# Kernel optimization log

Measured on AMD Instinct MI355X. Metric: run time of the kernel, lower is better.

## Reference

```python
import jax, jax.numpy as jnp
import numpy as np

N = 50000
E_RAND = 800000
F_IN = 128
H = 4          # num_heads
D_HID = 32     # hidden per-head dim
D_OUT = 32     # output per-head dim
NEG_SLOPE_ATTN = 0.2   # DGL GATConv attention leaky_relu
NEG_SLOPE_ACT = 0.01   # F.leaky_relu default activation


def setup_inputs() -> dict:
    key = jax.random.key(0)
    ks = jax.random.split(key, 12)
    x = jax.random.normal(ks[0], (N, F_IN), dtype=jnp.float32)
    src_r = jax.random.randint(ks[1], (E_RAND,), 0, N, dtype=jnp.int32)
    dst_r = jax.random.randint(ks[2], (E_RAND,), 0, N, dtype=jnp.int32)
    loop = jnp.arange(N, dtype=jnp.int32)
    src = jnp.concatenate([src_r, loop])  # add_self_loop
    dst = jnp.concatenate([dst_r, loop])
    sc1 = 1.0 / np.sqrt(F_IN)
    sc2 = 1.0 / np.sqrt(H * D_HID)
    W1 = jax.random.normal(ks[3], (F_IN, H * D_HID), dtype=jnp.float32) * sc1
    al1 = jax.random.normal(ks[4], (H, D_HID), dtype=jnp.float32) * sc1
    ar1 = jax.random.normal(ks[5], (H, D_HID), dtype=jnp.float32) * sc1
    b1 = jnp.zeros((H * D_HID,), dtype=jnp.float32)
    W2 = jax.random.normal(ks[6], (H * D_HID, H * D_OUT), dtype=jnp.float32) * sc2
    al2 = jax.random.normal(ks[7], (H, D_OUT), dtype=jnp.float32) * sc2
    ar2 = jax.random.normal(ks[8], (H, D_OUT), dtype=jnp.float32) * sc2
    b2 = jnp.zeros((H * D_OUT,), dtype=jnp.float32)
    return {"x": x, "src": src, "dst": dst,
            "W1": W1, "al1": al1, "ar1": ar1, "b1": b1,
            "W2": W2, "al2": al2, "ar2": ar2, "b2": b2}


def gat_conv(x, src, dst, W, al, ar, b, act_slope):
    n = x.shape[0]
    h, d = al.shape
    feat = (x @ W).reshape(n, h, d)                 # [N,H,D]
    el = jnp.einsum('nhd,hd->nh', feat, al)         # [N,H]
    er = jnp.einsum('nhd,hd->nh', feat, ar)
    # edge attention score on edge u->v: leaky_relu(el[u] + er[v])
    e = jax.nn.leaky_relu(el[src] + er[dst], NEG_SLOPE_ATTN)  # [E,H]
    # edge softmax over incoming edges of each dst node (self-loops guarantee >=1 edge)
    m = jax.ops.segment_max(e, dst, num_segments=n)           # [N,H]
    ex = jnp.exp(e - m[dst])
    s = jax.ops.segment_sum(ex, dst, num_segments=n)
    a = ex / s[dst]                                           # [E,H]
    # attention-weighted scatter-sum of source features
    out = jax.ops.segment_sum(a[:, :, None] * feat[src], dst, num_segments=n)  # [N,H,D]
    out = out + b.reshape(h, d)
    if act_slope is not None:
        out = jax.nn.leaky_relu(out, act_slope)
    return out.reshape(n, h * d)                    # flatten(1)


def reference(x, src, dst, W1, al1, ar1, b1, W2, al2, ar2, b2):
    h = gat_conv(x, src, dst, W1, al1, ar1, b1, NEG_SLOPE_ACT)
    out = gat_conv(h, src, dst, W2, al2, ar2, b2, None)  # last layer: no activation
    return out
```

## Files before the change

### kernel.cpp

```cpp
#include <hip/hip_runtime.h>
#include <hip/hip_bf16.h>
#include <hip/hip_fp16.h>

#define HEADS 4
#define DHEAD 32
#define FDIM 128
#define BCAP 64
#define RPB 64
#define XPAD (FDIM/4 + 1)
#define DEGPAD 16
#define WSTRIDE 68

typedef float nfloat4 __attribute__((ext_vector_type(4)));

__device__ __forceinline__ void gemm_body(
    const float* __restrict__ X, const float* __restrict__ W,
    const float* __restrict__ al, const float* __restrict__ ar,
    __half* __restrict__ feat, float* __restrict__ el, float* __restrict__ er,
    int n, float* Xs) {
    int r0 = blockIdx.x * RPB;
    int rowsLeft = n - r0; if (rowsLeft > RPB) rowsLeft = RPB;
    {
        nfloat4* xsw = (nfloat4*)Xs;
        const nfloat4* Xg = (const nfloat4*)(X + (size_t)r0 * FDIM);
        for (int i = threadIdx.x; i < RPB * (FDIM / 4); i += 256) {
            int row = i >> 5, c4 = i & 31;
            int sr = row < rowsLeft ? row : 0;
            xsw[row * XPAD + c4] =
                __builtin_nontemporal_load(&Xg[(size_t)sr * (FDIM / 4) + c4]);
        }
    }
    __syncthreads();

    int head = __builtin_amdgcn_readfirstlane(threadIdx.x >> 6);
    int lane = threadIdx.x & 63;
    int row = r0 + lane;
    bool valid = row < n;

    const float4* xs4 = (const float4*)Xs + (size_t)lane * XPAD;
    const float* wb = W + head * DHEAD;

    float acc[32];
#pragma unroll
    for (int j = 0; j < 32; j++) acc[j] = 0.f;

#pragma unroll 4
    for (int k4 = 0; k4 < FDIM / 4; k4++) {
        float4 a = xs4[k4];
#pragma unroll
        for (int kk = 0; kk < 4; kk++) {
            const float4* wr = (const float4*)(wb + (size_t)(k4 * 4 + kk) * FDIM);
            float s = (&a.x)[kk];
#pragma unroll
            for (int j4 = 0; j4 < 8; j4++) {
                float4 wv = wr[j4];
                acc[j4 * 4 + 0] += s * wv.x;
                acc[j4 * 4 + 1] += s * wv.y;
                acc[j4 * 4 + 2] += s * wv.z;
                acc[j4 * 4 + 3] += s * wv.w;
            }
        }
    }

    float elv = 0.f, erv = 0.f;
#pragma unroll
    for (int j = 0; j < 32; j++) {
        elv += acc[j] * al[head * DHEAD + j];
        erv += acc[j] * ar[head * DHEAD + j];
    }
    if (valid) {
        el[(size_t)row * HEADS + head] = elv;
        er[(size_t)row * HEADS + head] = erv;
    }

    if (valid) {
        union { __half2 h2[16]; uint4 u4[4]; } pk;
#pragma unroll
        for (int m = 0; m < 16; m++)
            pk.h2[m] = __floats2half2_rn(acc[2 * m], acc[2 * m + 1]);
        uint4* dstp = (uint4*)(feat + (size_t)row * FDIM + head * DHEAD);
#pragma unroll
        for (int t = 0; t < 4; t++) dstp[t] = pk.u4[t];
    }
}

__global__ __launch_bounds__(256) void k_gemm_l1(
    const float* __restrict__ X, const float* __restrict__ W,
    const float* __restrict__ al, const float* __restrict__ ar,
    __half* __restrict__ feat, float* __restrict__ el, float* __restrict__ er, int n,
    const int* __restrict__ esrc, const int* __restrict__ edst,
    int* __restrict__ degp, ushort* __restrict__ bucket, int E) {
    __shared__ float Xs[RPB * 4 * XPAD];

    {
        int nb = gridDim.x;
        int echunk = (E + nb - 1) / nb;
        int e0 = blockIdx.x * echunk;
        int e1 = e0 + echunk; if (e1 > E) e1 = E;
        for (int base = e0 + threadIdx.x; base < e1; base += 256 * 8) {
            int d[8], s[8], p[8];
#pragma unroll
            for (int j = 0; j < 8; j++) {
                int idx = base + j * 256;
                if (idx < e1) {
                    d[j] = __builtin_nontemporal_load(&edst[idx]);
                    s[j] = __builtin_nontemporal_load(&esrc[idx]);
                } else d[j] = -1;
            }
#pragma unroll
            for (int j = 0; j < 8; j++)
                if (d[j] >= 0) p[j] = atomicAdd(&degp[(size_t)d[j] * DEGPAD], 1);
#pragma unroll
            for (int j = 0; j < 8; j++)
                if (d[j] >= 0 && p[j] < BCAP)
                    bucket[((size_t)d[j] << 6) + p[j]] = (ushort)s[j];
        }
    }

    gemm_body(X, W, al, ar, feat, el, er, n, Xs);
}

__global__ __launch_bounds__(256) void k_gemm_l2(
    const float* __restrict__ X, const float* __restrict__ W,
    const float* __restrict__ al, const float* __restrict__ ar,
    __half* __restrict__ feat, float* __restrict__ el, float* __restrict__ er, int n) {
    __shared__ float Xs[RPB * 4 * XPAD];
    gemm_body(X, W, al, ar, feat, el, er, n, Xs);
}

__device__ __forceinline__ void agg_body(
    const ushort* __restrict__ bucket, const int* __restrict__ degp,
    const __half2* __restrict__ feat2h, const float* __restrict__ el,
    const float* __restrict__ er, const float* __restrict__ b,
    float* __restrict__ out, int n, int apply_act) {
    __shared__ float ws_all[4][HEADS * WSTRIDE];
    int wave = threadIdx.x >> 6;
    int node = blockIdx.x * 4 + wave;
    if (node >= n) return;
    node = __builtin_amdgcn_readfirstlane(node);
    int lane = threadIdx.x & 63;
    float* ws = ws_all[wave];

    int cnt = __builtin_amdgcn_readfirstlane(degp[(size_t)node * DEGPAD]);
    if (cnt > BCAP) cnt = BCAP;
    const ushort* bkt = bucket + ((size_t)node << 6);

    {
        int ph = lane >> 4;
        int sl = lane & 15;
        float ern = er[(size_t)node * HEADS + ph];
        int slot[4]; float ev[4];
#pragma unroll
        for (int bb = 0; bb < 4; bb++) {
            slot[bb] = bb * 16 + sl;
            int s = (int)bkt[slot[bb]];
            if (s >= n) s = 0;
            ev[bb] = el[(size_t)s * HEADS + ph];
        }
#pragma unroll
        for (int bb = 0; bb < 4; bb++) {
            float t = ev[bb] + ern;
            t = t > 0.f ? t : 0.2f * t;
            float w = (slot[bb] < cnt) ? __expf(t) : 0.f;
            ws[ph * WSTRIDE + slot[bb]] = w;
        }
    }
    asm volatile("s_waitcnt lgkmcnt(0)" ::: "memory");

    int h = lane >> 4;
    const float2* wsh2 = (const float2*)(ws + h * WSTRIDE);
    const uint* bp32 = (const uint*)bkt;
    float ax = 0.f, ay = 0.f, sw = 0.f;
    int pairs = (cnt + 1) >> 1;
    for (int k0 = 0; k0 < pairs; k0 += 4) {
        uint pk[4];
#pragma unroll
        for (int u = 0; u < 4; u++) {
            int kk = k0 + u;
            pk[u] = __builtin_amdgcn_readfirstlane(kk < pairs ? bp32[kk] : 0u);
        }
        __half2 f[8]; float2 w2[4];
#pragma unroll
        for (int u = 0; u < 4; u++) {
            int s0 = (int)(pk[u] & 0xffffu), s1 = (int)(pk[u] >> 16);
            if (s0 >= n) s0 = 0;
            if (s1 >= n) s1 = 0;
            f[2 * u]     = feat2h[(size_t)s0 * 64 + lane];
            f[2 * u + 1] = feat2h[(size_t)s1 * 64 + lane];
            w2[u] = wsh2[k0 + u];
        }
#pragma unroll
        for (int u = 0; u < 4; u++) {
            float2 f0 = __half22float2(f[2 * u]);
            float2 f1 = __half22float2(f[2 * u + 1]);
            sw += w2[u].x + w2[u].y;
            ax += w2[u].x * f0.x + w2[u].y * f1.x;
            ay += w2[u].x * f0.y + w2[u].y * f1.y;
        }
    }

    float inv = 1.0f / sw;
    float2 bv = ((const float2*)b)[lane];
    float ox = ax * inv + bv.x;
    float oy = ay * inv + bv.y;
    if (apply_act) {
        ox = ox > 0.f ? ox : 0.01f * ox;
        oy = oy > 0.f ? oy : 0.01f * oy;
    }
    float2 o; o.x = ox; o.y = oy;
    ((float2*)out)[(size_t)node * 64 + lane] = o;
}

__global__ __launch_bounds__(256) void k_agg_l1(
    const ushort* __restrict__ bucket, const int* __restrict__ degp,
    const __half2* __restrict__ feat2h, const float* __restrict__ el,
    const float* __restrict__ er, const float* __restrict__ b,
    float* __restrict__ out, int n) {
    agg_body(bucket, degp, feat2h, el, er, b, out, n, 1);
}

__global__ __launch_bounds__(256) void k_agg_l2(
    const ushort* __restrict__ bucket, const int* __restrict__ degp,
    const __half2* __restrict__ feat2h, const float* __restrict__ el,
    const float* __restrict__ er, const float* __restrict__ b,
    float* __restrict__ out, int n) {
    agg_body(bucket, degp, feat2h, el, er, b, out, n, 0);
}


extern "C" void kernel_launch(void* const* d_in, const int* in_sizes, int n_in,
                              void* d_out, int out_size, void* d_ws, size_t ws_size,
                              hipStream_t stream) {
    const float* x   = (const float*)d_in[0];
    const int*   src = (const int*)d_in[1];
    const int*   dst = (const int*)d_in[2];
    const float* W1  = (const float*)d_in[3];
    const float* al1 = (const float*)d_in[4];
    const float* ar1 = (const float*)d_in[5];
    const float* b1  = (const float*)d_in[6];
    const float* W2  = (const float*)d_in[7];
    const float* al2 = (const float*)d_in[8];
    const float* ar2 = (const float*)d_in[9];
    const float* b2  = (const float*)d_in[10];
    int N = in_sizes[0] / FDIM;
    int E = in_sizes[1];
    float* out = (float*)d_out;

    __half* featA  = (__half*)d_ws;
    float*  elb    = (float*)(featA + (size_t)N * FDIM);
    float*  erb    = elb + (size_t)N * HEADS;
    int*    degp   = (int*)(erb + (size_t)N * HEADS);
    ushort* bucket = (ushort*)(degp + (size_t)N * DEGPAD);
    float*  hbuf   = out;

    int gblocks = (N + RPB - 1) / RPB;
    int ablocks = (N + 3) / 4;

    (void)hipMemsetAsync(degp, 0, (size_t)N * DEGPAD * sizeof(int), stream);

    k_gemm_l1<<<gblocks, 256, 0, stream>>>(x, W1, al1, ar1, featA, elb, erb, N,
                                           src, dst, degp, bucket, E);
    k_agg_l1<<<ablocks, 256, 0, stream>>>(bucket, degp, (const __half2*)featA,
                                          elb, erb, b1, hbuf, N);

    k_gemm_l2<<<gblocks, 256, 0, stream>>>(hbuf, W2, al2, ar2, featA, elb, erb, N);
    k_agg_l2<<<ablocks, 256, 0, stream>>>(bucket, degp, (const __half2*)featA,
                                          elb, erb, b2, out, N);
}
```

Before: 274.5 us.

## Replace global-atomic edge bucketing with binned counting-sort pipeline

Graph construction switches from per-edge global atomics on a padded degree array to a three-pass binned counting sort. First a shared-memory histogram of destination bins, then a scan and a partition of packed (dst,src) edges into bins, then per-bin local-atomic bucket fill. The goal is to remove contended, scattered global atomics and the large memset of the padded degree array. In exchange it adds three small kernel launches and an extra pass over the edges, and it reuses the output buffer as scratch space. Packing dst in 16 bits only works because the low bits are recomputed per bin, and src must fit in 16 bits.

```diff
diff --git a/kernel.cpp b/kernel.cpp
--- a/kernel.cpp
+++ b/kernel.cpp
@@ -8,7 +8,8 @@
 #define BCAP 64
 #define RPB 64
 #define XPAD (FDIM/4 + 1)
-#define DEGPAD 16
+#define BINSH 8
+#define MAXBINS 256
 #define WSTRIDE 68
 
 typedef float nfloat4 __attribute__((ext_vector_type(4)));
@@ -88,48 +89,106 @@
     const float* __restrict__ X, const float* __restrict__ W,
     const float* __restrict__ al, const float* __restrict__ ar,
     __half* __restrict__ feat, float* __restrict__ el, float* __restrict__ er, int n,
-    const int* __restrict__ esrc, const int* __restrict__ edst,
-    int* __restrict__ degp, ushort* __restrict__ bucket, int E) {
+    const int* __restrict__ edst, int* __restrict__ bincnt, int E) {
     __shared__ float Xs[RPB * 4 * XPAD];
-
+    __shared__ int hist[MAXBINS];
+
+    for (int i = threadIdx.x; i < MAXBINS; i += 256) hist[i] = 0;
+    __syncthreads();
     {
         int nb = gridDim.x;
         int echunk = (E + nb - 1) / nb;
         int e0 = blockIdx.x * echunk;
         int e1 = e0 + echunk; if (e1 > E) e1 = E;
-        for (int base = e0 + threadIdx.x; base < e1; base += 256 * 8) {
-            int d[8], s[8], p[8];
-#pragma unroll
-            for (int j = 0; j < 8; j++) {
-                int idx = base + j * 256;
-                if (idx < e1) {
-                    d[j] = __builtin_nontemporal_load(&edst[idx]);
-                    s[j] = __builtin_nontemporal_load(&esrc[idx]);
-                } else d[j] = -1;
-            }
-#pragma unroll
-            for (int j = 0; j < 8; j++)
-                if (d[j] >= 0) p[j] = atomicAdd(&degp[(size_t)d[j] * DEGPAD], 1);
-#pragma unroll
-            for (int j = 0; j < 8; j++)
-                if (d[j] >= 0 && p[j] < BCAP)
-                    bucket[((size_t)d[j] << 6) + p[j]] = (ushort)s[j];
-        }
+        for (int idx = e0 + threadIdx.x; idx < e1; idx += 256)
+            atomicAdd(&hist[__builtin_nontemporal_load(&edst[idx]) >> BINSH], 1);
+        __syncthreads();
+        int hv = hist[threadIdx.x];
+        if (threadIdx.x < MAXBINS && hv) atomicAdd(&bincnt[threadIdx.x], hv);
     }
 
     gemm_body(X, W, al, ar, feat, el, er, n, Xs);
 }
 
-__global__ __launch_bounds__(256) void k_gemm_l2(
-    const float* __restrict__ X, const float* __restrict__ W,
-    const float* __restrict__ al, const float* __restrict__ ar,
-    __half* __restrict__ feat, float* __restrict__ el, float* __restrict__ er, int n) {
-    __shared__ float Xs[RPB * 4 * XPAD];
-    gemm_body(X, W, al, ar, feat, el, er, n, Xs);
+__global__ __launch_bounds__(256) void k_scan(
+    const int* __restrict__ bincnt, int* __restrict__ binbase,
+    int* __restrict__ cursor, int nbins) {
+    __shared__ int sb[MAXBINS];
+    int tid = threadIdx.x;
+    int v0 = (tid < nbins) ? bincnt[tid] : 0;
+    sb[tid] = v0;
+    __syncthreads();
+    for (int off = 1; off < MAXBINS; off <<= 1) {
+        int t = 0;
+        if (tid >= off) t = sb[tid - off];
+        __syncthreads();
+        if (tid >= off) sb[tid] += t;
+        __syncthreads();
+    }
+    int excl = sb[tid] - v0;
+    if (tid < nbins) { binbase[tid] = excl; cursor[tid] = excl; }
+    if (tid == 0) binbase[nbins] = sb[MAXBINS - 1];
+}
+
+__global__ __launch_bounds__(256) void k_p2(
+    const int* __restrict__ esrc, const int* __restrict__ edst,
+    int* __restrict__ cursor, uint* __restrict__ ebin, int E, int nbins) {
+    __shared__ int lcnt[MAXBINS];
+    __shared__ int lbase[MAXBINS];
+    int tid = threadIdx.x;
+    for (int i = tid; i < MAXBINS; i += 256) lcnt[i] = 0;
+    __syncthreads();
+    int nb = gridDim.x;
+    int echunk = (E + nb - 1) / nb;
+    int e0 = blockIdx.x * echunk;
+    int e1 = e0 + echunk; if (e1 > E) e1 = E;
+    int d[5], s[5], lo[5], bb[5];
+    bool v[5];
+#pragma unroll
+    for (int j = 0; j < 5; j++) {
+        int idx = e0 + j * 256 + tid;
+        v[j] = idx < e1;
+        if (v[j]) {
+            d[j] = __builtin_nontemporal_load(&edst[idx]);
+            s[j] = __builtin_nontemporal_load(&esrc[idx]);
+            bb[j] = d[j] >> BINSH;
+            lo[j] = atomicAdd(&lcnt[bb[j]], 1);
+        }
+    }
+    __syncthreads();
+    if (tid < nbins && lcnt[tid] > 0)
+        lbase[tid] = atomicAdd(&cursor[tid], lcnt[tid]);
+    __syncthreads();
+#pragma unroll
+    for (int j = 0; j < 5; j++)
+        if (v[j])
+            ebin[lbase[bb[j]] + lo[j]] = (uint)(d[j] & 0xffff) | ((uint)s[j] << 16);
+}
+
+__global__ __launch_bounds__(256) void k_p3(
+    const uint* __restrict__ ebin, const int* __restrict__ binbase,
+    ushort* __restrict__ bucket, int* __restrict__ deg, int n) {
+    __shared__ int ldeg[MAXBINS];
+    int tid = threadIdx.x;
+    ldeg[tid] = 0;
+    __syncthreads();
+    int bin = blockIdx.x;
+    int nb0 = bin << BINSH;
+    int lo = binbase[bin], hi = binbase[bin + 1];
+    for (int i = lo + tid; i < hi; i += 256) {
+        uint e = ebin[i];
+        int d = (int)(e & 0xffffu);
+        int s = (int)(e >> 16);
+        int slot = atomicAdd(&ldeg[d - nb0], 1);
+        if (slot < BCAP) bucket[((size_t)d << 6) + slot] = (ushort)s;
+    }
+    __syncthreads();
+    int node = nb0 + tid;
+    if (node < n) deg[node] = ldeg[tid];
 }
 
 __device__ __forceinline__ void agg_body(
-    const ushort* __restrict__ bucket, const int* __restrict__ degp,
+    const ushort* __restrict__ bucket, const int* __restrict__ deg,
     const __half2* __restrict__ feat2h, const float* __restrict__ el,
     const float* __restrict__ er, const float* __restrict__ b,
     float* __restrict__ out, int n, int apply_act) {
@@ -141,7 +200,7 @@
     int lane = threadIdx.x & 63;
     float* ws = ws_all[wave];
 
-    int cnt = __builtin_amdgcn_readfirstlane(degp[(size_t)node * DEGPAD]);
+    int cnt = __builtin_amdgcn_readfirstlane(deg[node]);
     if (cnt > BCAP) cnt = BCAP;
     const ushort* bkt = bucket + ((size_t)node << 6);
 
@@ -212,19 +271,27 @@
 }
 
 __global__ __launch_bounds__(256) void k_agg_l1(
-    const ushort* __restrict__ bucket, const int* __restrict__ degp,
+    const ushort* __restrict__ bucket, const int* __restrict__ deg,
     const __half2* __restrict__ feat2h, const float* __restrict__ el,
     const float* __restrict__ er, const float* __restrict__ b,
     float* __restrict__ out, int n) {
-    agg_body(bucket, degp, feat2h, el, er, b, out, n, 1);
+    agg_body(bucket, deg, feat2h, el, er, b, out, n, 1);
 }
 
 __global__ __launch_bounds__(256) void k_agg_l2(
-    const ushort* __restrict__ bucket, const int* __restrict__ degp,
+    const ushort* __restrict__ bucket, const int* __restrict__ deg,
     const __half2* __restrict__ feat2h, const float* __restrict__ el,
     const float* __restrict__ er, const float* __restrict__ b,
     float* __restrict__ out, int n) {
-    agg_body(bucket, degp, feat2h, el, er, b, out, n, 0);
+    agg_body(bucket, deg, feat2h, el, er, b, out, n, 0);
+}
+
+__global__ __launch_bounds__(256) void k_gemm_l2(
+    const float* __restrict__ X, const float* __restrict__ W,
+    const float* __restrict__ al, const float* __restrict__ ar,
+    __half* __restrict__ feat, float* __restrict__ el, float* __restrict__ er, int n) {
+    __shared__ float Xs[RPB * 4 * XPAD];
+    gemm_body(X, W, al, ar, feat, el, er, n, Xs);
 }
 
 
@@ -246,24 +313,34 @@
     int E = in_sizes[1];
     float* out = (float*)d_out;
 
-    __half* featA  = (__half*)d_ws;
-    float*  elb    = (float*)(featA + (size_t)N * FDIM);
-    float*  erb    = elb + (size_t)N * HEADS;
-    int*    degp   = (int*)(erb + (size_t)N * HEADS);
-    ushort* bucket = (ushort*)(degp + (size_t)N * DEGPAD);
-    float*  hbuf   = out;
+    __half* featA   = (__half*)d_ws;
+    float*  elb     = (float*)(featA + (size_t)N * FDIM);
+    float*  erb     = elb + (size_t)N * HEADS;
+    int*    deg     = (int*)(erb + (size_t)N * HEADS);
+    int*    bincnt  = deg + N;
+    int*    binbase = bincnt + MAXBINS;
+    int*    cursor  = binbase + MAXBINS + 1;
+    ushort* bucket  = (ushort*)(cursor + MAXBINS);
+    float*  hbuf    = out;
+    uint*   ebin    = (uint*)d_out;
 
     int gblocks = (N + RPB - 1) / RPB;
     int ablocks = (N + 3) / 4;
-
-    (void)hipMemsetAsync(degp, 0, (size_t)N * DEGPAD * sizeof(int), stream);
+    int nbins = (N + (1 << BINSH) - 1) >> BINSH;
+    int p2b = (E + 1279) / 1280;
+
+    (void)hipMemsetAsync(bincnt, 0, MAXBINS * sizeof(int), stream);
 
     k_gemm_l1<<<gblocks, 256, 0, stream>>>(x, W1, al1, ar1, featA, elb, erb, N,
-                                           src, dst, degp, bucket, E);
-    k_agg_l1<<<ablocks, 256, 0, stream>>>(bucket, degp, (const __half2*)featA,
+                                           dst, bincnt, E);
+    k_scan<<<1, 256, 0, stream>>>(bincnt, binbase, cursor, nbins);
+    k_p2<<<p2b, 256, 0, stream>>>(src, dst, cursor, ebin, E, nbins);
+    k_p3<<<nbins, 256, 0, stream>>>(ebin, binbase, bucket, deg, N);
+
+    k_agg_l1<<<ablocks, 256, 0, stream>>>(bucket, deg, (const __half2*)featA,
                                           elb, erb, b1, hbuf, N);
 
     k_gemm_l2<<<gblocks, 256, 0, stream>>>(hbuf, W2, al2, ar2, featA, elb, erb, N);
-    k_agg_l2<<<ablocks, 256, 0, stream>>>(bucket, degp, (const __half2*)featA,
+    k_agg_l2<<<ablocks, 256, 0, stream>>>(bucket, deg, (const __half2*)featA,
                                           elb, erb, b2, out, N);
 }
```

After: 278.6 us. About the same (+1.5%).
